# Kernel tuning notes

Measured on AMD Instinct MI355X. Metric: run time of the kernel, lower is better.

The kernel has to match this reference:

```python
import itertools
import jax
import jax.numpy as jnp
import numpy as np

FRAME_H, FRAME_W = 480, 640
HFOV = 79
CAM_H_CM = 88.0
NUM_SEM = 16
MAP_SIZE_CM, RES = 4800, 5
VR = 100
BEEN_CLOSE_CM = 200
GDS = 2
DU = 4
CAT_THR, EXP_THR, MAP_THR = 5.0, 1.0, 1.0
MIN_D_CM, MAX_D_CM = 50.0, 350.0
MIN_OBS_H_CM = 25
DIL_ITER, DIL_SIZE = 1, 3

NON_SEM = 4
LOCAL = MAP_SIZE_CM // GDS // RES
GLOBAL = MAP_SIZE_CM // RES
MAX_VH = int(360 / RES)
MIN_VH = int(-40 / RES)
ZB = MAX_VH - MIN_VH
MIN_Z = int(MIN_OBS_H_CM / RES - MIN_VH)
MAX_Z = int((CAM_H_CM + 1) / RES - MIN_VH)
XC = (FRAME_W - 1) / 2.0
ZC = (FRAME_H - 1) / 2.0
FOCAL = (FRAME_W / 2.0) / np.tan(np.deg2rad(HFOV / 2.0))
DEG = 57.29577951308232
B, T = 2, 4
C_MAP = NON_SEM + NUM_SEM

GPOSE0 = jnp.array([24.0, 24.0, 0.0], jnp.float32)
ORIG0 = jnp.array([12.0, 12.0, 0.0], jnp.float32)
LPOSE0 = GPOSE0 - ORIG0
LMB0 = jnp.array([240, 720, 240, 720], jnp.int32)

_XS = np.arange(FRAME_W, dtype=np.float32)[::DU]
_ZS = np.arange(FRAME_H - 1, -1, -1, dtype=np.float32)[::DU]


def point_cloud(depth):
    d = depth[:, ::DU, ::DU]
    valid = (d > MIN_D_CM) & (d < MAX_D_CM)
    X = (_XS[None, None, :] - XC) * d / FOCAL
    Z = (_ZS[None, :, None] - ZC) * d / FOCAL
    pts = jnp.stack([X, d, Z], -1).reshape(d.shape[0], -1, 3)
    return pts, valid.reshape(d.shape[0], -1)


def avg_pool(x, k):
    b, c, h, w = x.shape
    return x.reshape(b, c, h // k, k, w // k, k).mean((3, 5))


def splat(feat, coords):
    bs, fc, n = feat.shape
    dims = (VR, VR, ZB)
    G = VR * VR * ZB
    pos = [coords[:, d] * dims[d] / 2.0 + dims[d] / 2.0 for d in range(3)]
    fl = [jnp.floor(p) for p in pos]
    out = jnp.zeros((fc, bs * G), feat.dtype)
    offs = (jnp.arange(bs) * G)[:, None]
    for corner in itertools.product((0.0, 1.0), repeat=3):
        idx = jnp.zeros_like(pos[0])
        w = jnp.ones_like(pos[0])
        for d in range(3):
            p = fl[d] + corner[d]
            safe = ((p > 0) & (p < dims[d])).astype(feat.dtype)
            w = w * (1.0 - jnp.abs(pos[d] - p)) * safe
            idx = idx * dims[d] + p * safe
        flat = (idx.astype(jnp.int32) + offs).reshape(-1)
        vals = (feat * w[:, None, :]).transpose(1, 0, 2).reshape(fc, -1)
        out = out.at[:, flat].add(vals)
    out = jnp.round(out)
    return out.reshape(fc, bs, VR, VR, ZB).transpose(1, 0, 2, 3, 4)


def affine_grid(theta, h, w):
    ys = jnp.linspace(-1.0, 1.0, h)
    xs = jnp.linspace(-1.0, 1.0, w)
    gy, gx = jnp.meshgrid(ys, xs, indexing="ij")
    base = jnp.stack([gx, gy, jnp.ones_like(gx)], -1)
    return jnp.einsum("bij,hwj->bhwi", theta, base)


def _sample_one(im, grid):
    c, h, w = im.shape
    x = (grid[..., 0] + 1.0) * (w - 1) / 2.0
    y = (grid[..., 1] + 1.0) * (h - 1) / 2.0
    x0 = jnp.floor(x)
    y0 = jnp.floor(y)
    out = jnp.zeros((c,) + x.shape, im.dtype)
    for dx, dy in ((0, 0), (1, 0), (0, 1), (1, 1)):
        xi = x0 + dx
        yi = y0 + dy
        wgt = (1.0 - jnp.abs(x - xi)) * (1.0 - jnp.abs(y - yi))
        ok = (xi >= 0) & (xi <= w - 1) & (yi >= 0) & (yi <= h - 1)
        xi_c = jnp.clip(xi, 0, w - 1).astype(jnp.int32)
        yi_c = jnp.clip(yi, 0, h - 1).astype(jnp.int32)
        out = out + im[:, yi_c, xi_c] * (wgt * ok)[None]
    return out


grid_sample = jax.vmap(_sample_one)


def get_new_pose(pose, rel):
    s = jnp.sin(pose[:, 2] / DEG)
    c = jnp.cos(pose[:, 2] / DEG)
    x = pose[:, 0] + rel[:, 0] * c - rel[:, 1] * s
    y = pose[:, 1] + rel[:, 0] * s + rel[:, 1] * c
    o = pose[:, 2] + rel[:, 2] * DEG
    o = jnp.fmod(o - 180.0, 360.0) + 180.0
    o = jnp.fmod(o + 180.0, 360.0) - 180.0
    return jnp.stack([x, y, o], 1)


def update_local(obs, pdelta, prev_map, prev_pose):
    bs = obs.shape[0]
    pts, valid = point_cloud(obs[:, 3])
    pts = pts.at[..., 2].add(CAM_H_CM)
    pts = pts.at[..., 0].add(VR * RES / 2.0)
    cx = (pts[..., 0] / RES - VR // 2) / VR * 2.0
    cy = (pts[..., 1] / RES - VR // 2) / VR * 2.0
    cz = (pts[..., 2] / RES - (MAX_VH + MIN_VH) // 2) / ZB * 2.0
    coords = jnp.stack([cx, cy, cz], 1)
    coords = jnp.where(valid[:, None, :], coords, 2.0)
    sem = avg_pool(obs[:, 4:], DU).reshape(bs, NUM_SEM, -1)
    feat = jnp.concatenate([jnp.ones_like(sem[:, :1]), sem], 1)
    vox = splat(feat, coords)
    agent_h = vox[..., MIN_Z:MAX_Z].sum(-1)
    all_h = vox.sum(-1)
    fp_map = jnp.clip(agent_h[:, :1] / MAP_THR, 0.0, 1.0)
    fp_exp = jnp.clip(all_h[:, :1] / EXP_THR, 0.0, 1.0)
    sem_pred = jnp.clip(agent_h[:, 1:] / CAT_THR, 0.0, 1.0)
    x1 = LOCAL // 2 - VR // 2
    y1 = LOCAL // 2
    av = jnp.zeros((bs, C_MAP, LOCAL, LOCAL), obs.dtype)
    av = av.at[:, 0:1, y1:y1 + VR, x1:x1 + VR].set(fp_map)
    av = av.at[:, 1:2, y1:y1 + VR, x1:x1 + VR].set(fp_exp)
    av = av.at[:, NON_SEM:, y1:y1 + VR, x1:x1 + VR].set(sem_pred)
    pose = get_new_pose(prev_pose, pdelta)
    half = LOCAL // 2
    stx = -(pose[:, 0] * 100.0 / RES - half) / half
    sty = -(pose[:, 1] * 100.0 / RES - half) / half
    th = (90.0 - pose[:, 2]) * (np.pi / 180.0)
    ct, snt = jnp.cos(th), jnp.sin(th)
    zr, on = jnp.zeros_like(ct), jnp.ones_like(ct)
    th1 = jnp.stack([jnp.stack([ct, -snt, zr], -1), jnp.stack([snt, ct, zr], -1)], 1)
    th2 = jnp.stack([jnp.stack([on, zr, stx], -1), jnp.stack([zr, on, sty], -1)], 1)
    rotated = grid_sample(av, affine_grid(th1, LOCAL, LOCAL))
    translated = grid_sample(rotated, affine_grid(th2, LOCAL, LOCAL))
    cur = jnp.maximum(prev_map, translated)
    obst = cur[:, 0:1]
    kern = jnp.ones((1, 1, DIL_SIZE, DIL_SIZE), cur.dtype)
    for _ in range(DIL_ITER):
        obst = (jax.lax.conv(obst, kern, (1, 1), "SAME") > 0.5).astype(cur.dtype)
    cur = cur.at[:, 0].set(obst[:, 0])
    xg = (pose[:, 0] * 100.0 / RES).astype(jnp.int32)
    yg = (pose[:, 1] * 100.0 / RES).astype(jnp.int32)
    rr = jnp.arange(LOCAL)
    drow = rr[None, :, None] - yg[:, None, None]
    dcol = rr[None, None, :] - xg[:, None, None]
    sq = ((jnp.abs(drow) <= 2) & (jnp.abs(dcol) <= 2)).astype(cur.dtype)
    cur = cur.at[:, 2].set(sq)
    rad = BEEN_CLOSE_CM // RES
    disk = ((drow * drow + dcol * dcol) <= rad * rad).astype(cur.dtype)
    cur = cur.at[:, 3].set(jnp.maximum(cur[:, 3], disk))
    return cur, pose


def update_global_env(lmap, gmap, lpose, gpose, lmb, orig, updg):
    gpose_n = lpose + orig
    gmap_n = jax.lax.dynamic_update_slice(gmap, lmap, (0, lmb[0], lmb[2]))
    r = (gpose_n[1] * 100.0 / RES).astype(jnp.int32)
    c = (gpose_n[0] * 100.0 / RES).astype(jnp.int32)
    gx1 = jnp.clip(r - LOCAL // 2, 0, GLOBAL - LOCAL)
    gy1 = jnp.clip(c - LOCAL // 2, 0, GLOBAL - LOCAL)
    lmb_n = jnp.stack([gx1, gx1 + LOCAL, gy1, gy1 + LOCAL]).astype(jnp.int32)
    orig_n = jnp.stack([gy1 * RES / 100.0, gx1 * RES / 100.0, jnp.zeros(())]).astype(orig.dtype)
    lmap_n = jax.lax.dynamic_slice(gmap_n, (0, lmb_n[0], lmb_n[2]), lmap.shape)
    lpose_n = gpose_n - orig_n
    w = lambda a, b: jnp.where(updg, a, b)
    return (w(lmap_n, lmap), w(gmap_n, gmap), w(lpose_n, lpose),
            w(gpose_n, gpose), w(lmb_n, lmb), w(orig_n, orig))


def map_features(lmap, gmap):
    bs = gmap.shape[0]
    gdown = gmap[:, :NON_SEM].reshape(bs, NON_SEM, LOCAL, GDS, LOCAL, GDS).max((3, 5))
    return jnp.concatenate([lmap[:, :NON_SEM], gdown, lmap[:, NON_SEM:]], 1)


def forward(seq_obs, seq_pose_delta, seq_dones, seq_update_global, seq_camera_poses,
            init_local_map, init_global_map, init_local_pose, init_global_pose,
            init_lmb, init_origins):
    def step(carry, xs):
        lmap, gmap, lpose, gpose, lmb, orig = carry
        obs, pdelta, done, updg = xs
        d4 = done[:, None, None, None]
        d2 = done[:, None]
        lmap = jnp.where(d4, 0.0, lmap)
        gmap = jnp.where(d4, 0.0, gmap)
        lpose = jnp.where(d2, LPOSE0, lpose)
        gpose = jnp.where(d2, GPOSE0, gpose)
        lmb = jnp.where(d2, LMB0, lmb)
        orig = jnp.where(d2, ORIG0, orig)
        lmap, lpose = update_local(obs, pdelta, lmap, lpose)
        lmap, gmap, lpose, gpose, lmb, orig = jax.vmap(update_global_env)(
            lmap, gmap, lpose, gpose, lmb, orig, updg)
        feats = map_features(lmap, gmap)
        return (lmap, gmap, lpose, gpose, lmb, orig), (feats, lpose, gpose, lmb, orig)

    carry0 = (init_local_map, init_global_map, init_local_pose, init_global_pose,
              init_lmb, init_origins)
    xs = (jnp.swapaxes(seq_obs, 0, 1), jnp.swapaxes(seq_pose_delta, 0, 1),
          jnp.swapaxes(seq_dones, 0, 1), jnp.swapaxes(seq_update_global, 0, 1))
    (lmap, gmap, _, _, _, _), (fe, lp, gp, lb, og) = jax.lax.scan(step, carry0, xs)
    sw = lambda a: jnp.swapaxes(a, 0, 1)
    return sw(fe), lmap, gmap, sw(lp), sw(gp), sw(lb), sw(og)


def setup_inputs() -> dict:
    key = jax.random.key(0)
    ks = jax.random.split(key, 4)
    rgb = jax.random.uniform(ks[0], (B, T, 3, FRAME_H, FRAME_W), jnp.float32)
    depth = MIN_D_CM + jax.random.uniform(ks[1], (B, T, 1, FRAME_H, FRAME_W), jnp.float32) * (MAX_D_CM - MIN_D_CM + 100.0)
    seg = (jax.random.uniform(ks[2], (B, T, NUM_SEM, FRAME_H, FRAME_W)) > 0.95).astype(jnp.float32)
    seq_obs = jnp.concatenate([rgb, depth, seg], 2)
    seq_pose_delta = jax.random.normal(ks[3], (B, T, 3), jnp.float32) * jnp.array([0.25, 0.05, 0.1], jnp.float32)
    return {
        "seq_obs": seq_obs,
        "seq_pose_delta": seq_pose_delta,
        "seq_dones": jnp.zeros((B, T), bool),
        "seq_update_global": jnp.ones((B, T), bool),
        "seq_camera_poses": jnp.tile(jnp.eye(4, dtype=jnp.float32)[None], (B, 1, 1)),
        "init_local_map": jnp.zeros((B, C_MAP, LOCAL, LOCAL), jnp.float32),
        "init_global_map": jnp.zeros((B, C_MAP, GLOBAL, GLOBAL), jnp.float32),
        "init_local_pose": jnp.tile(LPOSE0[None], (B, 1)),
        "init_global_pose": jnp.tile(GPOSE0[None], (B, 1)),
        "init_lmb": jnp.tile(LMB0[None], (B, 1)),
        "init_origins": jnp.tile(ORIG0[None], (B, 1)),
    }


def reference(seq_obs, seq_pose_delta, seq_dones, seq_update_global, seq_camera_poses,
              init_local_map, init_global_map, init_local_pose, init_global_pose,
              init_lmb, init_origins):
    return forward(seq_obs, seq_pose_delta, seq_dones, seq_update_global, seq_camera_poses,
                   init_local_map, init_global_map, init_local_pose, init_global_pose,
                   init_lmb, init_origins)
```

## Files before the change

kernel.cpp:

```cpp
#include <hip/hip_runtime.h>
#include <math.h>


#define BB 2
#define TT 4
#define CMAP 20
#define LOC 480
#define GLOB 960
#define VOXC 17
#define NH 120
#define NW 160
#define NPTS (NH*NW)
#define LOC2 (LOC*LOC)
#define G2 (GLOB*GLOB)
#define FH 480
#define FW 640
#define LOCW 240
#define LOCW2 (LOCW*LOCW)
#define WOFF 120
#define CH0Z 69
#define SEMZ 12
#define CELLS 6100
#define CHSZ ((CH0Z + 16*SEMZ)*CELLS)

#define FE_OFF 0L
#define LM_OFF 44236800L
#define LM_SZ  9216000L
#define GM_OFF 53452800L
#define GM_SZ  36864000L
#define LP_OFF 90316800L
#define GP_OFF 90316824L
#define LB_OFF 90316848L
#define OG_OFF 90316880L

#define VOX_SZ   (2L*CHSZ)
#define RED_OFF  3184200L
#define TMP_OFF  3544200L
#define CUR_OFF  4005000L
#define PTF_OFF  13221000L
#define PTI_OFF  13221064L
#define GLIN_OFF 13221128L

__device__ __forceinline__ int iabs(int v){ return v<0? -v : v; }


__device__ __forceinline__ void glin_body(int i, float* glin){
    float g;
    if(i==LOC-1) g = 1.0f;
    else { float s = (float)i/479.0f; g = s - (1.0f - s); }
    glin[i] = g;
}

__device__ void poses_body(const float* ilp,const float* igp,
                           const int* ilmb,const float* iog,
                           const unsigned char* dones_raw,
                           const unsigned char* updg_raw,
                           const float* pdelta,
                           float* out,float* ptf,int* pti){
    #pragma clang fp contract(off)
    int stride;
    if(updg_raw[1]|updg_raw[2]|updg_raw[3]) stride = 1;
    else if(updg_raw[4])                    stride = 4;
    else                                    stride = 8;
    const float DEGF = 57.29577951308232f;
    for(int b=0;b<BB;b++){
        float lp0=ilp[b*3],lp1=ilp[b*3+1],lp2=ilp[b*3+2];
        float gp0=igp[b*3],gp1=igp[b*3+1],gp2=igp[b*3+2];
        float og0=iog[b*3],og1=iog[b*3+1],og2=iog[b*3+2];
        int m0=ilmb[b*4],m1=ilmb[b*4+1],m2=ilmb[b*4+2],m3=ilmb[b*4+3];
        for(int t=0;t<TT;t++){
            int dn = dones_raw[(b*TT+t)*stride]!=0;
            int ug = updg_raw[(b*TT+t)*stride]!=0;
            if(dn){
                lp0=12.f;lp1=12.f;lp2=0.f; gp0=24.f;gp1=24.f;gp2=0.f;
                og0=12.f;og1=12.f;og2=0.f; m0=240;m1=720;m2=240;m3=720;
            }
            float r0=pdelta[(b*TT+t)*3+0], r1=pdelta[(b*TT+t)*3+1], r2=pdelta[(b*TT+t)*3+2];
            float s=sinf(lp2/DEGF), c=cosf(lp2/DEGF);
            float x = lp0 + r0*c - r1*s;
            float y = lp1 + r0*s + r1*c;
            float o = lp2 + r2*DEGF;
            o = fmodf(o-180.f,360.f)+180.f;
            o = fmodf(o+180.f,360.f)-180.f;
            lp0=x; lp1=y; lp2=o;
            float th = (90.0f - o) * (float)(M_PI/180.0);
            float ct = cosf(th), snt = sinf(th);
            float ax = (lp0*100.0f)/5.0f;
            float ay = (lp1*100.0f)/5.0f;
            float stx = -((ax-240.0f)/240.0f);
            float sty = -((ay-240.0f)/240.0f);
            float* pf = ptf + (size_t)(t*BB+b)*8;
            pf[0]=lp0; pf[1]=lp1; pf[2]=o; pf[3]=ct; pf[4]=snt; pf[5]=stx; pf[6]=sty;
            int* pi = pti + (size_t)(t*BB+b)*8;
            pi[0]=m0; pi[1]=m2;
            pi[4]=(int)ax; pi[5]=(int)ay;
            pi[6]=dn; pi[7]=ug;
            float g0=lp0+og0, g1=lp1+og1, g2=lp2+og2;
            if(ug){
                int r  = (int)((g1*100.0f)/5.0f);
                int cc = (int)((g0*100.0f)/5.0f);
                int gx1 = min(max(r-240,0),480);
                int gy1 = min(max(cc-240,0),480);
                m0=gx1; m1=gx1+480; m2=gy1; m3=gy1+480;
                float o0 = ((float)gy1*5.0f)/100.0f;
                float o1 = ((float)gx1*5.0f)/100.0f;
                og0=o0; og1=o1; og2=0.f;
                lp0=g0-o0; lp1=g1-o1; lp2=g2;
                gp0=g0; gp1=g1; gp2=g2;
            }
            pi[2]=m0; pi[3]=m2;
            out[LP_OFF+(b*TT+t)*3+0]=lp0; out[LP_OFF+(b*TT+t)*3+1]=lp1; out[LP_OFF+(b*TT+t)*3+2]=lp2;
            out[GP_OFF+(b*TT+t)*3+0]=gp0; out[GP_OFF+(b*TT+t)*3+1]=gp1; out[GP_OFF+(b*TT+t)*3+2]=gp2;
            out[OG_OFF+(b*TT+t)*3+0]=og0; out[OG_OFF+(b*TT+t)*3+1]=og1; out[OG_OFF+(b*TT+t)*3+2]=og2;
            out[LB_OFF+(b*TT+t)*4+0]=(float)m0; out[LB_OFF+(b*TT+t)*4+1]=(float)m1;
            out[LB_OFF+(b*TT+t)*4+2]=(float)m2; out[LB_OFF+(b*TT+t)*4+3]=(float)m3;
        }
    }
}

__device__ __forceinline__ void splat_body(int tid,const float* __restrict__ obs,int t,
                                           float* __restrict__ vox,float FOCAL){
    #pragma clang fp contract(off)
    int p  = tid % NPTS;
    int ch = (tid/NPTS) % VOXC;
    int b  = tid / (VOXC*NPTS);
    int zi = p / NW, xi = p % NW;
    const float* ob = obs + ((size_t)(b*TT+t))*CMAP*FH*FW;
    float d = ob[3*FH*FW + (size_t)(4*zi)*FW + 4*xi];
    if(!(d>50.0f && d<350.0f)) return;
    float f;
    if(ch==0) f = 1.0f;
    else{
        const float* cp = ob + (size_t)(4+ch-1)*FH*FW + (size_t)(4*zi)*FW + 4*xi;
        float s=0.f;
        #pragma unroll
        for(int r=0;r<4;r++){
            float4 v = *(const float4*)(cp + (size_t)r*FW);
            s += v.x+v.y+v.z+v.w;
        }
        f = s*0.0625f;
    }
    float X  = ((float)(4*xi) - 319.5f)*d/FOCAL;
    float Zc = ((float)(479-4*zi) - 239.5f)*d/FOCAL;
    float p0f = X + 250.0f;
    float p1f = d;
    float p2f = Zc + 88.0f;
    float cx = (p0f/5.0f - 50.0f)/100.0f*2.0f;
    float cy = (p1f/5.0f - 50.0f)/100.0f*2.0f;
    float cz = (p2f/5.0f - 32.0f)/80.0f*2.0f;
    float pos0 = cx*100.0f/2.0f + 50.0f;
    float pos1 = cy*100.0f/2.0f + 50.0f;
    float pos2 = cz*80.0f/2.0f + 40.0f;
    float f0=floorf(pos0), f1=floorf(pos1), f2=floorf(pos2);
    float* base = vox + (size_t)b*CHSZ;
    #pragma unroll
    for(int c0=0;c0<2;c0++){
        float q0=f0+(float)c0;
        if(!(q0>0.f && q0<100.f)) continue;
        float w0 = 1.0f-fabsf(pos0-q0);
        int iq0 = (int)q0;
        #pragma unroll
        for(int c1=0;c1<2;c1++){
            float q1=f1+(float)c1;
            if(!(q1>=10.0f && q1<=70.0f)) continue;
            float w1 = w0*(1.0f-fabsf(pos1-q1));
            int cell = iq0*61 + ((int)q1-10);
            #pragma unroll
            for(int c2=0;c2<2;c2++){
                float q2=f2+(float)c2;
                if(!(q2>0.f && q2<70.f)) continue;
                int iq2 = (int)q2;
                float w = w1*(1.0f-fabsf(pos2-q2));
                if(ch==0)
                    atomicAdd(base + (size_t)(iq2-1)*CELLS + cell, w);
                else if(iq2>=13 && iq2<25)
                    atomicAdd(base + (size_t)(CH0Z + (ch-1)*SEMZ + (iq2-13))*CELLS + cell, f*w);
            }
        }
    }
}

__device__ __forceinline__ void reduce_body(int tid,float* __restrict__ vox,float* __restrict__ red){
    int cell = tid % 10000;
    int ch   = (tid/10000) % VOXC;
    int b    = tid / (VOXC*10000);
    int q0 = cell/100, q1 = cell%100;
    float allh=0.f, ag=0.f;
    if(q1>=10 && q1<=70){
        float* base = vox + (size_t)b*CHSZ;
        if(ch==0){
            float* vp = base + q0*61 + (q1-10);
            for(int z=0;z<CH0Z;z++){
                float v = rintf(vp[(size_t)z*CELLS]);
                allh += v;
                if(z>=12 && z<24) ag += v;
                vp[(size_t)z*CELLS] = 0.0f;
            }
        }else{
            float* vp = base + (size_t)(CH0Z + (ch-1)*SEMZ)*CELLS + q0*61 + (q1-10);
            for(int z=0;z<SEMZ;z++){
                float v = rintf(vp[(size_t)z*CELLS]);
                ag += v;
                vp[(size_t)z*CELLS] = 0.0f;
            }
        }
    }
    float* rb = red + (size_t)b*18*10000;
    if(ch==0){
        rb[cell]       = fminf(fmaxf(ag,0.f),1.f);
        rb[10000+cell] = fminf(fmaxf(allh,0.f),1.f);
    }else{
        rb[(ch+1)*10000+cell] = fminf(fmaxf(ag/5.0f,0.f),1.f);
    }
}

__device__ void transf_body(int tid,const float* __restrict__ red,
                            const float* __restrict__ ptf,const int* __restrict__ pti,
                            const float* __restrict__ glin,int t,
                            const float* __restrict__ P,
                            float* __restrict__ C,float* __restrict__ tmp0){
    #pragma clang fp contract(off)
    int x = tid % LOC;
    int y = (tid/LOC) % LOC;
    int b = tid / LOC2;
    const float* pf = ptf + (size_t)(t*BB+b)*8;
    const int*   pi = pti + (size_t)(t*BB+b)*8;
    float ct = pf[3], snt = pf[4], stx = pf[5], sty = pf[6];
    float xs = (glin[x]+stx+1.0f)*239.5f;
    float ys = (glin[y]+sty+1.0f)*239.5f;
    float x0=floorf(xs), y0=floorf(ys);
    float tw[4]; int ro[4][4]; float rw[4][4];
    #pragma unroll
    for(int k=0;k<4;k++){
        float xi = x0 + (float)(k&1), yi = y0 + (float)(k>>1);
        float wgt = (1.0f-fabsf(xs-xi))*(1.0f-fabsf(ys-yi));
        int xii=(int)xi, yii=(int)yi;
        bool ok = !(xi<0.f||xi>479.f||yi<0.f||yi>479.f)
                  && xii>=WOFF && xii<WOFF+LOCW && yii>=WOFF && yii<WOFF+LOCW;
        tw[k] = ok ? wgt : 0.0f;
        if(ok){
            float gx2 = glin[xii], gy2 = glin[yii];
            float grx = ct*gx2 - snt*gy2;
            float gry = snt*gx2 + ct*gy2;
            float rxs = (grx+1.0f)*239.5f;
            float rys = (gry+1.0f)*239.5f;
            float rx0 = floorf(rxs), ry0 = floorf(rys);
            #pragma unroll
            for(int j=0;j<4;j++){
                float xj = rx0 + (float)(j&1), yj = ry0 + (float)(j>>1);
                float rwgt = (1.0f-fabsf(rxs-xj))*(1.0f-fabsf(rys-yj));
                int xjj=(int)xj, yjj=(int)yj;
                bool okj = !(xj<0.f||xj>479.f||yj<0.f||yj>479.f)
                           && yjj>=240 && yjj<340 && xjj>=190 && xjj<290;
                rw[k][j] = okj ? rwgt : 0.0f;
                ro[k][j] = okj ? (yjj-240)*100 + (xjj-190) : 0;
            }
        }else{
            #pragma unroll
            for(int j=0;j<4;j++){ rw[k][j]=0.0f; ro[k][j]=0; }
        }
    }
    int xg=pi[4], yg=pi[5];
    float sq   = (iabs(y-yg)<=2 && iabs(x-xg)<=2) ? 1.0f : 0.0f;
    int dr=y-yg, dc=x-xg;
    float disk = (dr*dr+dc*dc <= 1600) ? 1.0f : 0.0f;
    const float* rb = red + (size_t)b*18*10000;
    size_t pix = (size_t)y*LOC + x;
    const float* Pb = P + (size_t)b*CMAP*LOC2 + pix;
    float* Cb = C + (size_t)b*CMAP*LOC2 + pix;
    for(int c=0;c<CMAP;c++){
        if(c==2){ Cb[2*LOC2] = sq; continue; }
        if(c==3){ Cb[3*LOC2] = fmaxf(Pb[3*LOC2], disk); continue; }
        int wc = (c<2) ? c : c-2;
        const float* rc = rb + (size_t)wc*10000;
        float rv0 = rc[ro[0][0]]*rw[0][0]; rv0 += rc[ro[0][1]]*rw[0][1];
        rv0 += rc[ro[0][2]]*rw[0][2];      rv0 += rc[ro[0][3]]*rw[0][3];
        float rv1 = rc[ro[1][0]]*rw[1][0]; rv1 += rc[ro[1][1]]*rw[1][1];
        rv1 += rc[ro[1][2]]*rw[1][2];      rv1 += rc[ro[1][3]]*rw[1][3];
        float rv2 = rc[ro[2][0]]*rw[2][0]; rv2 += rc[ro[2][1]]*rw[2][1];
        rv2 += rc[ro[2][2]]*rw[2][2];      rv2 += rc[ro[2][3]]*rw[2][3];
        float rv3 = rc[ro[3][0]]*rw[3][0]; rv3 += rc[ro[3][1]]*rw[3][1];
        rv3 += rc[ro[3][2]]*rw[3][2];      rv3 += rc[ro[3][3]]*rw[3][3];
        float acc = rv0*tw[0]; acc += rv1*tw[1]; acc += rv2*tw[2]; acc += rv3*tw[3];
        float res = fmaxf(Pb[(size_t)c*LOC2], acc);
        if(c==0) tmp0[(size_t)b*LOC2 + pix] = res;
        else     Cb[(size_t)c*LOC2] = res;
    }
}

__device__ __forceinline__ float dil_at(const float* __restrict__ tb,int y,int x){
    float s=0.f;
    for(int dy=-1;dy<=1;dy++){
        int yy=y+dy; if(yy<0||yy>=LOC) continue;
        for(int dx=-1;dx<=1;dx++){
            int xx=x+dx; if(xx<0||xx>=LOC) continue;
            s += tb[(size_t)yy*LOC+xx];
        }
    }
    return (s>0.5f)?1.0f:0.0f;
}

__device__ void outf_body(int tid,const float* __restrict__ C,const float* __restrict__ tmp0,
                          float* __restrict__ gmap,float* __restrict__ P,float* __restrict__ fe,
                          const int* __restrict__ pti,int t){
    int x = tid % LOC;
    int y = (tid/LOC) % LOC;
    int b = tid / LOC2;
    const int* pi = pti + (size_t)(t*BB+b)*8;
    int r0o=pi[0], c0o=pi[1], r0n=pi[2], c0n=pi[3];
    int ug = pi[7];
    size_t pix = (size_t)y*LOC + x;
    const float* Cb = C + (size_t)b*CMAP*LOC2;
    const float* tb = tmp0 + (size_t)b*LOC2;
    float* gB = gmap + (size_t)b*CMAP*G2;
    float* pB = P + (size_t)b*CMAP*LOC2;
    float* feB = fe + ((size_t)(b*TT+t))*24*LOC2;
    if(ug){
        size_t gp = (size_t)(r0o+y)*GLOB + (c0o+x);
        gB[gp] = dil_at(tb,y,x);
        for(int c=1;c<CMAP;c++)
            gB[(size_t)c*G2 + gp] = Cb[(size_t)c*LOC2 + pix];
    }
    int dr = ug ? (r0n - r0o) : 0;
    int dc = ug ? (c0n - c0o) : 0;
    int sy = y + dr, sx = x + dc;
    bool inT = (sy>=0 && sy<LOC && sx>=0 && sx<LOC);
    size_t gpn = ug ? ((size_t)(r0n+y)*GLOB + (c0n+x)) : 0;
    size_t spix = (size_t)sy*LOC + sx;
    for(int c=0;c<CMAP;c++){
        float v;
        if(inT) v = (c==0) ? dil_at(tb,sy,sx) : Cb[(size_t)c*LOC2 + spix];
        else    v = gB[(size_t)c*G2 + gpn];
        pB[(size_t)c*LOC2 + pix] = v;
        int fc = (c<4) ? c : c+4;
        feB[(size_t)fc*LOC2 + pix] = v;
    }
    for(int gc=0;gc<4;gc++){
        float m = 0.f; bool first = true;
        #pragma unroll
        for(int dy=0;dy<2;dy++){
            #pragma unroll
            for(int dx=0;dx<2;dx++){
                int ty = 2*y+dy, tx = 2*x+dx;
                int ly = ty - r0o, lx = tx - c0o;
                float tv;
                if(ug && ly>=0 && ly<LOC && lx>=0 && lx<LOC)
                    tv = (gc==0) ? dil_at(tb,ly,lx)
                                 : Cb[(size_t)gc*LOC2 + (size_t)ly*LOC + lx];
                else
                    tv = gB[(size_t)gc*G2 + (size_t)ty*GLOB + tx];
                m = first ? tv : fmaxf(m, tv);
                first = false;
            }
        }
        feB[(size_t)(4+gc)*LOC2 + pix] = m;
    }
}


__global__ __launch_bounds__(256) void k_init(float4* __restrict__ vox,
                                              float4* __restrict__ lmap,float4* __restrict__ gmap,
                                              const float* ilp,const float* igp,
                                              const int* ilmb,const float* iog,
                                              const unsigned char* dones_raw,const unsigned char* updg_raw,
                                              const float* pdelta,float* out,
                                              float* ptf,int* pti,float* glin){
    long i = (long)blockIdx.x*blockDim.x + threadIdx.x;
    if(blockIdx.x==0){
        if(threadIdx.x < LOC) glin_body((int)threadIdx.x, glin);
        if(threadIdx.x == 0)
            poses_body(ilp,igp,ilmb,iog,dones_raw,updg_raw,pdelta,out,ptf,pti);
    }
    const long NV4 = VOX_SZ/4, L4 = LM_SZ/4, G4 = GM_SZ/4;
    const long total = NV4+L4+G4;
    float4 z; z.x=0.f;z.y=0.f;z.z=0.f;z.w=0.f;
    long st = (long)gridDim.x*blockDim.x;
    for(long k=i;k<total;k+=st){
        if(k<NV4) vox[k]=z;
        else if(k<NV4+L4) lmap[k-NV4]=z;
        else gmap[k-NV4-L4]=z;
    }
}

__global__ __launch_bounds__(256) void k_reset(float4* __restrict__ lmap,float4* __restrict__ gmap,
                                               const int* __restrict__ pti,int t){
    const long L4 = (long)CMAP*LOC2/4, G4 = (long)CMAP*G2/4, per = L4+G4;
    bool d0 = pti[(size_t)(t*BB+0)*8+6]!=0, d1 = pti[(size_t)(t*BB+1)*8+6]!=0;
    long total = (d0?per:0)+(d1?per:0);
    if(total==0) return;
    float4 z; z.x=0.f;z.y=0.f;z.z=0.f;z.w=0.f;
    long i = (long)blockIdx.x*blockDim.x + threadIdx.x;
    long st = (long)gridDim.x*blockDim.x;
    for(long k=i;k<total;k+=st){
        long r = k; int b;
        if(d0){ if(r<per) b=0; else { b=1; r-=per; } } else b=1;
        if(r<L4) lmap[b*L4+r]=z; else gmap[b*G4+(r-L4)]=z;
    }
}

__global__ __launch_bounds__(256) void k_splat(const float* __restrict__ obs,int t,
                                               float* __restrict__ vox,float FOCAL){
    int tid = blockIdx.x*blockDim.x + threadIdx.x;
    if(tid >= BB*VOXC*NPTS) return;
    splat_body(tid,obs,t,vox,FOCAL);
}

__global__ __launch_bounds__(256) void k_reduce(float* __restrict__ vox,float* __restrict__ red){
    int tid = blockIdx.x*blockDim.x + threadIdx.x;
    if(tid >= BB*VOXC*10000) return;
    reduce_body(tid,vox,red);
}

__global__ __launch_bounds__(256) void k_transf(const float* __restrict__ red,
                                                const float* __restrict__ ptf,const int* __restrict__ pti,
                                                const float* __restrict__ glin,int t,
                                                const float* __restrict__ P,
                                                float* __restrict__ C,float* __restrict__ tmp0,
                                                const float* __restrict__ obs,
                                                float* __restrict__ vox,float FOCAL,int tnext){
    int NT  = (int)(gridDim.x*blockDim.x);
    int tid = (int)(blockIdx.x*blockDim.x + threadIdx.x);
    if(tnext>=0)
        for(int i=tid;i<BB*VOXC*NPTS;i+=NT) splat_body(i,obs,tnext,vox,FOCAL);
    if(tid >= BB*LOC2) return;
    transf_body(tid,red,ptf,pti,glin,t,P,C,tmp0);
}

__global__ __launch_bounds__(256) void k_outf(const float* __restrict__ C,const float* __restrict__ tmp0,
                                              float* __restrict__ gmap,float* __restrict__ P,
                                              float* __restrict__ fe,
                                              const int* __restrict__ pti,int t,
                                              float* __restrict__ vox,float* __restrict__ red,int tnext){
    int NT  = (int)(gridDim.x*blockDim.x);
    int tid = (int)(blockIdx.x*blockDim.x + threadIdx.x);
    if(tnext>=0)
        for(int i=tid;i<BB*VOXC*10000;i+=NT) reduce_body(i,vox,red);
    if(tid >= BB*LOC2) return;
    outf_body(tid,C,tmp0,gmap,P,fe,pti,t);
}

extern "C" void kernel_launch(void* const* d_in, const int* in_sizes, int n_in,
                              void* d_out, int out_size, void* d_ws, size_t ws_size,
                              hipStream_t stream){
    const float* obs    = (const float*)d_in[0];
    const float* pdelta = (const float*)d_in[1];
    const unsigned char* dones_raw = (const unsigned char*)d_in[2];
    const unsigned char* updg_raw  = (const unsigned char*)d_in[3];
    const float* ilp  = (const float*)d_in[7];
    const float* igp  = (const float*)d_in[8];
    const int*   ilmb = (const int*)d_in[9];
    const float* iog  = (const float*)d_in[10];

    float* out  = (float*)d_out;
    float* fe   = out + FE_OFF;
    float* lmap = out + LM_OFF;
    float* gmap = out + GM_OFF;

    float* wsf  = (float*)d_ws;
    float* vox  = wsf;
    float* red  = wsf + RED_OFF;
    float* tmp0 = wsf + TMP_OFF;
    float* curm = wsf + CUR_OFF;
    float* ptf  = wsf + PTF_OFF;
    int*   pti  = (int*)(wsf + PTI_OFF);
    float* glin = wsf + GLIN_OFF;

    const float FOCAL = (float)(320.0 / tan(39.5 * M_PI / 180.0));

    k_init<<<2048,256,0,stream>>>((float4*)vox,(float4*)lmap,(float4*)gmap,
                                  ilp,igp,ilmb,iog,dones_raw,updg_raw,pdelta,
                                  out,ptf,pti,glin);
    { int n=BB*VOXC*NPTS;  k_splat <<<(n+255)/256,256,0,stream>>>(obs,0,vox,FOCAL); }
    { int n=BB*VOXC*10000; k_reduce<<<(n+255)/256,256,0,stream>>>(vox,red); }

    const int nPix = BB*LOC2;
    for(int t=0;t<TT;t++){
        k_reset<<<2048,256,0,stream>>>((float4*)lmap,(float4*)gmap,pti,t);
        int tnext = (t+1<TT) ? t+1 : -1;
        k_transf<<<nPix/256,256,0,stream>>>(red,ptf,pti,glin,t,lmap,curm,tmp0,
                                            obs,vox,FOCAL,tnext);
        k_outf  <<<nPix/256,256,0,stream>>>(curm,tmp0,gmap,lmap,fe,pti,t,
                                            vox,red,tnext);
    }
}
```

Measured before the change: 1.065 ms.

## Write transformed local map directly into global map and fuse reset with reduce

```diff
diff --git a/kernel.cpp b/kernel.cpp
--- a/kernel.cpp
+++ b/kernel.cpp
@@ -217,7 +217,7 @@
 __device__ void transf_body(int tid,const float* __restrict__ red,
                             const float* __restrict__ ptf,const int* __restrict__ pti,
                             const float* __restrict__ glin,int t,
-                            const float* __restrict__ P,
+                            const float* __restrict__ P,float* __restrict__ gmap,
                             float* __restrict__ C,float* __restrict__ tmp0){
     #pragma clang fp contract(off)
     int x = tid % LOC;
@@ -264,27 +264,34 @@
     float sq   = (iabs(y-yg)<=2 && iabs(x-xg)<=2) ? 1.0f : 0.0f;
     int dr=y-yg, dc=x-xg;
     float disk = (dr*dr+dc*dc <= 1600) ? 1.0f : 0.0f;
+    int ug = pi[7];
+    int r0o = pi[0], c0o = pi[1];
     const float* rb = red + (size_t)b*18*10000;
     size_t pix = (size_t)y*LOC + x;
     const float* Pb = P + (size_t)b*CMAP*LOC2 + pix;
-    float* Cb = C + (size_t)b*CMAP*LOC2 + pix;
+    float* dstG = gmap + (size_t)b*CMAP*G2 + (size_t)(r0o+y)*GLOB + (c0o+x);
+    float* dstC = C + (size_t)b*CMAP*LOC2 + pix;
     for(int c=0;c<CMAP;c++){
-        if(c==2){ Cb[2*LOC2] = sq; continue; }
-        if(c==3){ Cb[3*LOC2] = fmaxf(Pb[3*LOC2], disk); continue; }
-        int wc = (c<2) ? c : c-2;
-        const float* rc = rb + (size_t)wc*10000;
-        float rv0 = rc[ro[0][0]]*rw[0][0]; rv0 += rc[ro[0][1]]*rw[0][1];
-        rv0 += rc[ro[0][2]]*rw[0][2];      rv0 += rc[ro[0][3]]*rw[0][3];
-        float rv1 = rc[ro[1][0]]*rw[1][0]; rv1 += rc[ro[1][1]]*rw[1][1];
-        rv1 += rc[ro[1][2]]*rw[1][2];      rv1 += rc[ro[1][3]]*rw[1][3];
-        float rv2 = rc[ro[2][0]]*rw[2][0]; rv2 += rc[ro[2][1]]*rw[2][1];
-        rv2 += rc[ro[2][2]]*rw[2][2];      rv2 += rc[ro[2][3]]*rw[2][3];
-        float rv3 = rc[ro[3][0]]*rw[3][0]; rv3 += rc[ro[3][1]]*rw[3][1];
-        rv3 += rc[ro[3][2]]*rw[3][2];      rv3 += rc[ro[3][3]]*rw[3][3];
-        float acc = rv0*tw[0]; acc += rv1*tw[1]; acc += rv2*tw[2]; acc += rv3*tw[3];
-        float res = fmaxf(Pb[(size_t)c*LOC2], acc);
-        if(c==0) tmp0[(size_t)b*LOC2 + pix] = res;
-        else     Cb[(size_t)c*LOC2] = res;
+        float v;
+        if(c==2)      v = sq;
+        else if(c==3) v = fmaxf(Pb[3*LOC2], disk);
+        else{
+            int wc = (c<2) ? c : c-2;
+            const float* rc = rb + (size_t)wc*10000;
+            float rv0 = rc[ro[0][0]]*rw[0][0]; rv0 += rc[ro[0][1]]*rw[0][1];
+            rv0 += rc[ro[0][2]]*rw[0][2];      rv0 += rc[ro[0][3]]*rw[0][3];
+            float rv1 = rc[ro[1][0]]*rw[1][0]; rv1 += rc[ro[1][1]]*rw[1][1];
+            rv1 += rc[ro[1][2]]*rw[1][2];      rv1 += rc[ro[1][3]]*rw[1][3];
+            float rv2 = rc[ro[2][0]]*rw[2][0]; rv2 += rc[ro[2][1]]*rw[2][1];
+            rv2 += rc[ro[2][2]]*rw[2][2];      rv2 += rc[ro[2][3]]*rw[2][3];
+            float rv3 = rc[ro[3][0]]*rw[3][0]; rv3 += rc[ro[3][1]]*rw[3][1];
+            rv3 += rc[ro[3][2]]*rw[3][2];      rv3 += rc[ro[3][3]]*rw[3][3];
+            float acc = rv0*tw[0]; acc += rv1*tw[1]; acc += rv2*tw[2]; acc += rv3*tw[3];
+            v = fmaxf(Pb[(size_t)c*LOC2], acc);
+        }
+        if(c==0){ tmp0[(size_t)b*LOC2 + pix] = v; continue; }
+        if(ug) dstG[(size_t)c*G2] = v;
+        else   dstC[(size_t)c*LOC2] = v;
     }
 }
 
@@ -310,50 +317,67 @@
     int r0o=pi[0], c0o=pi[1], r0n=pi[2], c0n=pi[3];
     int ug = pi[7];
     size_t pix = (size_t)y*LOC + x;
-    const float* Cb = C + (size_t)b*CMAP*LOC2;
     const float* tb = tmp0 + (size_t)b*LOC2;
     float* gB = gmap + (size_t)b*CMAP*G2;
     float* pB = P + (size_t)b*CMAP*LOC2;
     float* feB = fe + ((size_t)(b*TT+t))*24*LOC2;
     if(ug){
-        size_t gp = (size_t)(r0o+y)*GLOB + (c0o+x);
-        gB[gp] = dil_at(tb,y,x);
-        for(int c=1;c<CMAP;c++)
-            gB[(size_t)c*G2 + gp] = Cb[(size_t)c*LOC2 + pix];
-    }
-    int dr = ug ? (r0n - r0o) : 0;
-    int dc = ug ? (c0n - c0o) : 0;
-    int sy = y + dr, sx = x + dc;
-    bool inT = (sy>=0 && sy<LOC && sx>=0 && sx<LOC);
-    size_t gpn = ug ? ((size_t)(r0n+y)*GLOB + (c0n+x)) : 0;
-    size_t spix = (size_t)sy*LOC + sx;
-    for(int c=0;c<CMAP;c++){
-        float v;
-        if(inT) v = (c==0) ? dil_at(tb,sy,sx) : Cb[(size_t)c*LOC2 + spix];
-        else    v = gB[(size_t)c*G2 + gpn];
-        pB[(size_t)c*LOC2 + pix] = v;
-        int fc = (c<4) ? c : c+4;
-        feB[(size_t)fc*LOC2 + pix] = v;
-    }
-    for(int gc=0;gc<4;gc++){
-        float m = 0.f; bool first = true;
-        #pragma unroll
-        for(int dy=0;dy<2;dy++){
+        gB[(size_t)(r0o+y)*GLOB + (c0o+x)] = dil_at(tb,y,x);
+        int dr = r0n - r0o, dc = c0n - c0o;
+        int sy = y + dr, sx = x + dc;
+        bool inT = (sy>=0 && sy<LOC && sx>=0 && sx<LOC);
+        size_t gpn = (size_t)(r0n+y)*GLOB + (c0n+x);
+        for(int c=0;c<CMAP;c++){
+            float v;
+            if(c==0) v = inT ? dil_at(tb,sy,sx) : gB[gpn];
+            else     v = gB[(size_t)c*G2 + gpn];
+            pB[(size_t)c*LOC2 + pix] = v;
+            int fc = (c<4) ? c : c+4;
+            feB[(size_t)fc*LOC2 + pix] = v;
+        }
+        for(int gc=0;gc<4;gc++){
+            float m = 0.f; bool first = true;
             #pragma unroll
-            for(int dx=0;dx<2;dx++){
-                int ty = 2*y+dy, tx = 2*x+dx;
-                int ly = ty - r0o, lx = tx - c0o;
-                float tv;
-                if(ug && ly>=0 && ly<LOC && lx>=0 && lx<LOC)
-                    tv = (gc==0) ? dil_at(tb,ly,lx)
-                                 : Cb[(size_t)gc*LOC2 + (size_t)ly*LOC + lx];
-                else
-                    tv = gB[(size_t)gc*G2 + (size_t)ty*GLOB + tx];
-                m = first ? tv : fmaxf(m, tv);
-                first = false;
-            }
-        }
-        feB[(size_t)(4+gc)*LOC2 + pix] = m;
+            for(int dy=0;dy<2;dy++){
+                #pragma unroll
+                for(int dx=0;dx<2;dx++){
+                    int ty = 2*y+dy, tx = 2*x+dx;
+                    float tv;
+                    if(gc==0){
+                        int ly = ty - r0o, lx = tx - c0o;
+                        if(ly>=0 && ly<LOC && lx>=0 && lx<LOC) tv = dil_at(tb,ly,lx);
+                        else tv = gB[(size_t)ty*GLOB + tx];
+                    }else{
+                        tv = gB[(size_t)gc*G2 + (size_t)ty*GLOB + tx];
+                    }
+                    m = first ? tv : fmaxf(m, tv);
+                    first = false;
+                }
+            }
+            feB[(size_t)(4+gc)*LOC2 + pix] = m;
+        }
+    }else{
+        const float* Cb = C + (size_t)b*CMAP*LOC2;
+        for(int c=0;c<CMAP;c++){
+            float v = (c==0) ? dil_at(tb,y,x) : Cb[(size_t)c*LOC2 + pix];
+            pB[(size_t)c*LOC2 + pix] = v;
+            int fc = (c<4) ? c : c+4;
+            feB[(size_t)fc*LOC2 + pix] = v;
+        }
+        for(int gc=0;gc<4;gc++){
+            float m = 0.f; bool first = true;
+            #pragma unroll
+            for(int dy=0;dy<2;dy++){
+                #pragma unroll
+                for(int dx=0;dx<2;dx++){
+                    int ty = 2*y+dy, tx = 2*x+dx;
+                    float tv = gB[(size_t)gc*G2 + (size_t)ty*GLOB + tx];
+                    m = first ? tv : fmaxf(m, tv);
+                    first = false;
+                }
+            }
+            feB[(size_t)(4+gc)*LOC2 + pix] = m;
+        }
     }
 }
 
@@ -365,15 +389,15 @@
                                               const unsigned char* dones_raw,const unsigned char* updg_raw,
                                               const float* pdelta,float* out,
                                               float* ptf,int* pti,float* glin){
-    long i = (long)blockIdx.x*blockDim.x + threadIdx.x;
     if(blockIdx.x==0){
-        if(threadIdx.x < LOC) glin_body((int)threadIdx.x, glin);
+        for(int i=threadIdx.x;i<LOC;i+=blockDim.x) glin_body(i, glin);
         if(threadIdx.x == 0)
             poses_body(ilp,igp,ilmb,iog,dones_raw,updg_raw,pdelta,out,ptf,pti);
     }
     const long NV4 = VOX_SZ/4, L4 = LM_SZ/4, G4 = GM_SZ/4;
     const long total = NV4+L4+G4;
     float4 z; z.x=0.f;z.y=0.f;z.z=0.f;z.w=0.f;
+    long i = (long)blockIdx.x*blockDim.x + threadIdx.x;
     long st = (long)gridDim.x*blockDim.x;
     for(long k=i;k<total;k+=st){
         if(k<NV4) vox[k]=z;
@@ -382,22 +406,6 @@
     }
 }
 
-__global__ __launch_bounds__(256) void k_reset(float4* __restrict__ lmap,float4* __restrict__ gmap,
-                                               const int* __restrict__ pti,int t){
-    const long L4 = (long)CMAP*LOC2/4, G4 = (long)CMAP*G2/4, per = L4+G4;
-    bool d0 = pti[(size_t)(t*BB+0)*8+6]!=0, d1 = pti[(size_t)(t*BB+1)*8+6]!=0;
-    long total = (d0?per:0)+(d1?per:0);
-    if(total==0) return;
-    float4 z; z.x=0.f;z.y=0.f;z.z=0.f;z.w=0.f;
-    long i = (long)blockIdx.x*blockDim.x + threadIdx.x;
-    long st = (long)gridDim.x*blockDim.x;
-    for(long k=i;k<total;k+=st){
-        long r = k; int b;
-        if(d0){ if(r<per) b=0; else { b=1; r-=per; } } else b=1;
-        if(r<L4) lmap[b*L4+r]=z; else gmap[b*G4+(r-L4)]=z;
-    }
-}
-
 __global__ __launch_bounds__(256) void k_splat(const float* __restrict__ obs,int t,
                                                float* __restrict__ vox,float FOCAL){
     int tid = blockIdx.x*blockDim.x + threadIdx.x;
@@ -405,16 +413,29 @@
     splat_body(tid,obs,t,vox,FOCAL);
 }
 
-__global__ __launch_bounds__(256) void k_reduce(float* __restrict__ vox,float* __restrict__ red){
-    int tid = blockIdx.x*blockDim.x + threadIdx.x;
-    if(tid >= BB*VOXC*10000) return;
-    reduce_body(tid,vox,red);
+__global__ __launch_bounds__(256) void k_resred(float4* __restrict__ lmap,float4* __restrict__ gmap,
+                                                const int* __restrict__ pti,int t,
+                                                float* __restrict__ vox,float* __restrict__ red){
+    int NT  = (int)(gridDim.x*blockDim.x);
+    int tid = (int)(blockIdx.x*blockDim.x + threadIdx.x);
+    const long L4 = (long)CMAP*LOC2/4, G4 = (long)CMAP*G2/4, per = L4+G4;
+    bool d0 = pti[(size_t)(t*BB+0)*8+6]!=0, d1 = pti[(size_t)(t*BB+1)*8+6]!=0;
+    long totalr = (d0?per:0)+(d1?per:0);
+    if(totalr){
+        float4 z; z.x=0.f;z.y=0.f;z.z=0.f;z.w=0.f;
+        for(long k=tid;k<totalr;k+=NT){
+            long r = k; int b;
+            if(d0){ if(r<per) b=0; else { b=1; r-=per; } } else b=1;
+            if(r<L4) lmap[b*L4+r]=z; else gmap[b*G4+(r-L4)]=z;
+        }
+    }
+    for(int i=tid;i<BB*VOXC*10000;i+=NT) reduce_body(i,vox,red);
 }
 
 __global__ __launch_bounds__(256) void k_transf(const float* __restrict__ red,
                                                 const float* __restrict__ ptf,const int* __restrict__ pti,
                                                 const float* __restrict__ glin,int t,
-                                                const float* __restrict__ P,
+                                                const float* __restrict__ P,float* __restrict__ gmap,
                                                 float* __restrict__ C,float* __restrict__ tmp0,
                                                 const float* __restrict__ obs,
                                                 float* __restrict__ vox,float FOCAL,int tnext){
@@ -423,18 +444,14 @@
     if(tnext>=0)
         for(int i=tid;i<BB*VOXC*NPTS;i+=NT) splat_body(i,obs,tnext,vox,FOCAL);
     if(tid >= BB*LOC2) return;
-    transf_body(tid,red,ptf,pti,glin,t,P,C,tmp0);
+    transf_body(tid,red,ptf,pti,glin,t,P,gmap,C,tmp0);
 }
 
 __global__ __launch_bounds__(256) void k_outf(const float* __restrict__ C,const float* __restrict__ tmp0,
                                               float* __restrict__ gmap,float* __restrict__ P,
                                               float* __restrict__ fe,
-                                              const int* __restrict__ pti,int t,
-                                              float* __restrict__ vox,float* __restrict__ red,int tnext){
-    int NT  = (int)(gridDim.x*blockDim.x);
+                                              const int* __restrict__ pti,int t){
     int tid = (int)(blockIdx.x*blockDim.x + threadIdx.x);
-    if(tnext>=0)
-        for(int i=tid;i<BB*VOXC*10000;i+=NT) reduce_body(i,vox,red);
     if(tid >= BB*LOC2) return;
     outf_body(tid,C,tmp0,gmap,P,fe,pti,t);
 }
@@ -470,16 +487,14 @@
     k_init<<<2048,256,0,stream>>>((float4*)vox,(float4*)lmap,(float4*)gmap,
                                   ilp,igp,ilmb,iog,dones_raw,updg_raw,pdelta,
                                   out,ptf,pti,glin);
-    { int n=BB*VOXC*NPTS;  k_splat <<<(n+255)/256,256,0,stream>>>(obs,0,vox,FOCAL); }
-    { int n=BB*VOXC*10000; k_reduce<<<(n+255)/256,256,0,stream>>>(vox,red); }
+    { int n=BB*VOXC*NPTS; k_splat<<<(n+255)/256,256,0,stream>>>(obs,0,vox,FOCAL); }
 
     const int nPix = BB*LOC2;
     for(int t=0;t<TT;t++){
-        k_reset<<<2048,256,0,stream>>>((float4*)lmap,(float4*)gmap,pti,t);
+        { int n=BB*VOXC*10000; k_resred<<<(n+255)/256,256,0,stream>>>((float4*)lmap,(float4*)gmap,pti,t,vox,red); }
         int tnext = (t+1<TT) ? t+1 : -1;
-        k_transf<<<nPix/256,256,0,stream>>>(red,ptf,pti,glin,t,lmap,curm,tmp0,
+        k_transf<<<nPix/256,256,0,stream>>>(red,ptf,pti,glin,t,lmap,gmap,curm,tmp0,
                                             obs,vox,FOCAL,tnext);
-        k_outf  <<<nPix/256,256,0,stream>>>(curm,tmp0,gmap,lmap,fe,pti,t,
-                                            vox,red,tnext);
-    }
-}
+        k_outf  <<<nPix/256,256,0,stream>>>(curm,tmp0,gmap,lmap,fe,pti,t);
+    }
+}
```

Result: no change. 1.063 ms (-0.2%).
